# Performance work log

Measured on AMD Instinct MI355X. Metric: run time of the kernel, lower is better.

## Reference

```python
import jax, jax.numpy as jnp
import numpy as np

# Model dims (match init_kwargs / input_specs)
T, N, E, F_IN, F_OUT, BW = 16, 50000, 131072, 64, 64, 3


def setup_inputs() -> dict:
    key = jax.random.key(0)
    ks = jax.random.split(key, 6)
    x = jax.random.normal(ks[0], (T, N, F_IN), dtype=jnp.float32)
    M = jax.random.normal(ks[1], (T, T), dtype=jnp.float32)
    adj_rows = jax.random.randint(ks[2], (T, E), 0, N, dtype=jnp.int32)
    adj_cols = jax.random.randint(ks[3], (T, E), 0, N, dtype=jnp.int32)
    adj_vals = jax.random.uniform(ks[4], (T, E), dtype=jnp.float32)
    lim = float(np.sqrt(6.0 / (F_IN + F_OUT)))  # xavier_uniform
    weight = jax.random.uniform(ks[5], (F_IN, F_OUT), minval=-lim, maxval=lim, dtype=jnp.float32)
    return {"x": x, "M": M, "adj_vals": adj_vals, "weight": weight,
            "adj_rows": adj_rows, "adj_cols": adj_cols}


def _spmm(vals, rows, cols, x):
    # COO sparse [N,N] @ dense [N,F]: gather source rows, scatter-add to dest rows.
    return jax.ops.segment_sum(vals[:, None] * x[cols], rows, num_segments=x.shape[0])


def reference(x, M, adj_vals, weight, adj_rows, adj_cols):
    Tn, Nn, F = x.shape
    # Xt = M @ X (full M, as in compute_AtXt)
    Xt = (M @ x.reshape(Tn, -1)).reshape(Tn, Nn, F)
    k_idx = jnp.arange(Tn)
    AtXt = jnp.zeros((Tn, Nn, F), dtype=x.dtype)
    # Banded combination: At[k] = sum_{d=0}^{BW-1, k-d>=0} M[k, k-d] * A[k-d]
    # so At[k] @ Xt[k] = sum_d M[k,k-d] * (A[k-d] @ Xt[k])  -- avoids materializing At.
    for d in range(BW):
        j = k_idx - d
        valid = j >= 0
        jc = jnp.maximum(j, 0)
        w = jnp.where(valid, M[k_idx, jc], 0.0)  # [T] banded weights
        contrib = jax.vmap(_spmm)(adj_vals[jc], adj_rows[jc], adj_cols[jc], Xt)  # [T,N,F]
        AtXt = AtXt + w[:, None, None] * contrib
    # dropout is identity in eval mode; final dense projection
    return AtXt @ weight  # [T, N, F_OUT]
```

## Files before the change

kernel.cpp:

```cpp
#include <hip/hip_runtime.h>

#define TT 16
#define NN 50000
#define FF 64
#define EE 131072
#define NEDGE (TT*EE)
#define RPB 32
#define NRANGE ((NN + RPB - 1) / RPB)
#define NSUB 8
#define BCAP 256
#define NBUCK (NRANGE*NSUB)
#define SLOTS (NSUB*BCAP)
#define EMAX 1791
#define TAILI (EMAX*2)
#define APPBLKS (NEDGE/256)

typedef __attribute__((ext_vector_type(8))) short bf16x8;
typedef __attribute__((ext_vector_type(4))) short bf16x4;
typedef __attribute__((ext_vector_type(4))) float f32x4;
typedef __attribute__((ext_vector_type(2))) int   i32x2;
typedef __attribute__((ext_vector_type(2))) unsigned u32x2;

__device__ __forceinline__ unsigned pack2bf(float a, float b) {
    unsigned ua = __float_as_uint(a) + 0x8000u;
    unsigned ub = __float_as_uint(b) + 0x8000u;
    return __builtin_amdgcn_perm(ub, ua, 0x07060302u);
}
__device__ __forceinline__ float lo16f(unsigned u) { return __uint_as_float(u << 16); }
__device__ __forceinline__ float hi16f(unsigned u) { return __uint_as_float(u & 0xFFFF0000u); }

union U8 { unsigned u[4]; bf16x8 v; };
union U4 { unsigned u[2]; bf16x4 v; };

__device__ __forceinline__ f32x4 mfma16x16x16bf16(bf16x4 a, bf16x4 b, f32x4 c) {
#if __has_builtin(__builtin_amdgcn_mfma_f32_16x16x16bf16_1k)
    return __builtin_amdgcn_mfma_f32_16x16x16bf16_1k(a, b, c, 0, 0, 0);
#elif __has_builtin(__builtin_amdgcn_mfma_f32_16x16x16_bf16)
    return __builtin_amdgcn_mfma_f32_16x16x16_bf16(a, b, c, 0, 0, 0);
#else
    f32x4 d;
    asm volatile("v_mfma_f32_16x16x16_bf16 %0, %1, %2, %3\n\ts_nop 7\n\ts_nop 7"
                 : "=&v"(d) : "v"(a), "v"(b), "v"(c));
    return d;
#endif
}

__global__ __launch_bounds__(256) void k1_proj_mix(
    const float* __restrict__ x, const float* __restrict__ M,
    const float* __restrict__ W, unsigned short* __restrict__ Yt)
{
    const int tid  = threadIdx.x;
    const int wid  = tid >> 6;
    const int lane = tid & 63;
    const int col  = lane & 15;
    const int grp  = lane >> 4;

    bf16x8 bw[2][4];
#pragma unroll
    for (int q = 0; q < 2; ++q)
#pragma unroll
        for (int t = 0; t < 4; ++t) {
            U8 w8;
#pragma unroll
            for (int p = 0; p < 4; ++p)
                w8.u[p] = pack2bf(W[(q*32 + grp*8 + 2*p)*FF + t*16 + col],
                                  W[(q*32 + grp*8 + 2*p + 1)*FF + t*16 + col]);
            bw[q][t] = w8.v;
        }

    U4 m4;
    m4.u[0] = pack2bf(M[col*16 + grp*4 + 0], M[col*16 + grp*4 + 1]);
    m4.u[1] = pack2bf(M[col*16 + grp*4 + 2], M[col*16 + grp*4 + 3]);
    const bf16x4 mf = m4.v;

    const f32x4 zero = {0.f, 0.f, 0.f, 0.f};
    const int nwaves = gridDim.x * 4;

    for (int node = blockIdx.x*4 + wid; node < NN; node += nwaves) {
        const float* xb = x + (size_t)col*NN*FF + (size_t)node*FF + grp*8;
        float4 v0 = *reinterpret_cast<const float4*>(xb);
        float4 v1 = *reinterpret_cast<const float4*>(xb + 4);
        float4 v2 = *reinterpret_cast<const float4*>(xb + 32);
        float4 v3 = *reinterpret_cast<const float4*>(xb + 36);
        U8 a0, a1;
        a0.u[0] = pack2bf(v0.x, v0.y); a0.u[1] = pack2bf(v0.z, v0.w);
        a0.u[2] = pack2bf(v1.x, v1.y); a0.u[3] = pack2bf(v1.z, v1.w);
        a1.u[0] = pack2bf(v2.x, v2.y); a1.u[1] = pack2bf(v2.z, v2.w);
        a1.u[2] = pack2bf(v3.x, v3.y); a1.u[3] = pack2bf(v3.z, v3.w);

        f32x4 acc[4];
#pragma unroll
        for (int t = 0; t < 4; ++t) acc[t] = zero;
#pragma unroll
        for (int t = 0; t < 4; ++t)
            acc[t] = __builtin_amdgcn_mfma_f32_16x16x32_bf16(a0.v, bw[0][t], acc[t], 0, 0, 0);
#pragma unroll
        for (int t = 0; t < 4; ++t)
            acc[t] = __builtin_amdgcn_mfma_f32_16x16x32_bf16(a1.v, bw[1][t], acc[t], 0, 0, 0);

#pragma unroll
        for (int t = 0; t < 4; ++t) {
            U4 pb;
            pb.u[0] = pack2bf(acc[t][0], acc[t][1]);
            pb.u[1] = pack2bf(acc[t][2], acc[t][3]);
            f32x4 y = mfma16x16x16bf16(pb.v, mf, zero);
            u32x2 st;
            st[0] = pack2bf(y[0], y[1]);
            st[1] = pack2bf(y[2], y[3]);
            *reinterpret_cast<u32x2*>(Yt + (size_t)node*1024 + col*64 + t*16 + grp*4) = st;
        }
    }
}

__global__ __launch_bounds__(256) void append_kernel(
    const int* __restrict__ rows, const int* __restrict__ cols,
    const float* __restrict__ vals, int* __restrict__ bcnt,
    i32x2* __restrict__ btmp)
{
    const int i = blockIdx.x*256 + threadIdx.x;
    const int r = rows[i];
    const int j = i >> 17;
    const int b = (r >> 5)*NSUB + (blockIdx.x & 7);
    const int pos = atomicAdd(&bcnt[b], 1);
    if (pos < BCAP) {
        i32x2 e;
        e[0] = cols[i] | (((r & 31)*16 + j) << 16);
        e[1] = __float_as_int(vals[i]);
        btmp[(size_t)b*BCAP + pos] = e;
    }
}

__global__ __launch_bounds__(256) void sort_kernel(
    const int* __restrict__ bcnt, i32x2* __restrict__ btmp)
{
    __shared__ i32x2 sbuf[SLOTS];
    __shared__ int scnt[512], soff[512], scur[512], pscan[256];

    const int tid = threadIdx.x;
    const int blk = blockIdx.x;
    i32x2* region = btmp + (size_t)blk*SLOTS;

    scnt[tid] = 0; scnt[tid + 256] = 0;
    __syncthreads();

    int bc[NSUB]; i32x2 ent[NSUB];
#pragma unroll
    for (int s = 0; s < NSUB; ++s) {
        int c = bcnt[blk*NSUB + s];
        bc[s] = c < BCAP ? c : BCAP;
    }
#pragma unroll
    for (int s = 0; s < NSUB; ++s)
        if (tid < bc[s]) {
            ent[s] = region[s*BCAP + tid];
            atomicAdd(&scnt[((unsigned)ent[s][0]) >> 16], 1);
        }
    __syncthreads();

    const int a0 = scnt[2*tid], a1 = scnt[2*tid + 1];
    const int ps = a0 + a1;
    pscan[tid] = ps;
    __syncthreads();
    for (int o = 1; o < 256; o <<= 1) {
        int v = (tid >= o) ? pscan[tid - o] : 0;
        __syncthreads();
        pscan[tid] += v;
        __syncthreads();
    }
    const int excl = pscan[tid] - ps;
    soff[2*tid] = excl;      soff[2*tid + 1] = excl + a0;
    scur[2*tid] = excl;      scur[2*tid + 1] = excl + a0;
    __syncthreads();

#pragma unroll
    for (int s = 0; s < NSUB; ++s)
        if (tid < bc[s]) {
            const int key = ((unsigned)ent[s][0]) >> 16;
            const int pos = atomicAdd(&scur[key], 1);
            i32x2 se; se[0] = ent[s][0] & 0xFFFF; se[1] = ent[s][1];
            sbuf[pos] = se;
        }
    __syncthreads();

    const int total = soff[511] + scnt[511];
    const int lim = total < EMAX ? total : EMAX;
    for (int i = tid; i < lim; i += 256) region[i] = sbuf[i];
    int* tail = (int*)region + TAILI;
    tail[tid] = soff[tid];
    tail[tid + 256] = soff[tid + 256];
    if (tid == 0) tail[512] = lim;
}

template<int J>
__device__ __forceinline__ void k2_batch(int p0, int nj, int sbase, int esub, int fq,
    const i32x2* eb, const unsigned short* __restrict__ Yt,
    const float* __restrict__ M, f32x4* acc)
{
    const int p = p0 + esub;
    const bool act = p < nj;
    const int li = act ? (sbase + p) : 0;
    const i32x2 ent = eb[li];
    const float v = act ? __int_as_float(ent[1]) : 0.f;
    const int node = act ? ent[0] : 0;
    const unsigned short* yb = Yt + (size_t)node*1024 + J*64 + fq*4;
    {
        const u32x2 uv = *reinterpret_cast<const u32x2*>(yb);
        const float wv = M[J*17] * v;
        acc[J][0] = fmaf(wv, lo16f(uv[0]), acc[J][0]);
        acc[J][1] = fmaf(wv, hi16f(uv[0]), acc[J][1]);
        acc[J][2] = fmaf(wv, lo16f(uv[1]), acc[J][2]);
        acc[J][3] = fmaf(wv, hi16f(uv[1]), acc[J][3]);
    }
    if constexpr (J < 15) {
        const u32x2 uv = *reinterpret_cast<const u32x2*>(yb + 64);
        const float wv = M[J*17 + 16] * v;
        acc[J+1][0] = fmaf(wv, lo16f(uv[0]), acc[J+1][0]);
        acc[J+1][1] = fmaf(wv, hi16f(uv[0]), acc[J+1][1]);
        acc[J+1][2] = fmaf(wv, lo16f(uv[1]), acc[J+1][2]);
        acc[J+1][3] = fmaf(wv, hi16f(uv[1]), acc[J+1][3]);
    }
    if constexpr (J < 14) {
        const u32x2 uv = *reinterpret_cast<const u32x2*>(yb + 128);
        const float wv = M[J*17 + 32] * v;
        acc[J+2][0] = fmaf(wv, lo16f(uv[0]), acc[J+2][0]);
        acc[J+2][1] = fmaf(wv, hi16f(uv[0]), acc[J+2][1]);
        acc[J+2][2] = fmaf(wv, lo16f(uv[1]), acc[J+2][2]);
        acc[J+2][3] = fmaf(wv, hi16f(uv[1]), acc[J+2][3]);
    }
}

__global__ __launch_bounds__(256) void k2_gather(
    const unsigned short* __restrict__ Yt, const float* __restrict__ M,
    const i32x2* __restrict__ btmp, float* __restrict__ out)
{
    __shared__ i32x2 ebuf[4][128];
    const int tid  = threadIdx.x;
    const int wid  = tid >> 6;
    const int lane = tid & 63;
    const int esub = lane >> 4;
    const int fq   = lane & 15;
    const int r   = blockIdx.x*4 + wid;
    const int blk = r >> 5;
    const int rl  = r & 31;

    const i32x2* region = btmp + (size_t)blk*SLOTS;
    const int* tail = (const int*)region + TAILI;
    int o_l = 0;
    if (lane < 17) o_l = tail[rl*16 + lane];
    int off[17];
#pragma unroll
    for (int j = 0; j < 17; ++j) off[j] = __builtin_amdgcn_readlane(o_l, j);
    int ntot = off[16] - off[0];
    ntot = ntot < 128 ? ntot : 128;
    const i32x2* rowsrc = region + off[0];

    i32x2* eb = ebuf[wid];
    if (lane < ntot)      eb[lane]      = rowsrc[lane];
    if (lane + 64 < ntot) eb[lane + 64] = rowsrc[lane + 64];

    int c[16], sb[16];
#pragma unroll
    for (int j = 0; j < 16; ++j) {
        c[j]  = off[j+1] - off[j];
        sb[j] = off[j] - off[0];
    }

    f32x4 acc[16];
#pragma unroll
    for (int k = 0; k < 16; ++k) acc[k] = (f32x4){0.f, 0.f, 0.f, 0.f};

#define P1(J) k2_batch<J>(0, c[J], sb[J], esub, fq, eb, Yt, M, acc);
    P1(0)  P1(1)  P1(2)  P1(3)  P1(4)  P1(5)  P1(6)  P1(7)
    P1(8)  P1(9)  P1(10) P1(11) P1(12) P1(13) P1(14) P1(15)
#undef P1
#define P2(J) for (int p0 = 4; p0 < c[J]; p0 += 4) \
        k2_batch<J>(p0, c[J], sb[J], esub, fq, eb, Yt, M, acc);
    P2(0)  P2(1)  P2(2)  P2(3)  P2(4)  P2(5)  P2(6)  P2(7)
    P2(8)  P2(9)  P2(10) P2(11) P2(12) P2(13) P2(14) P2(15)
#undef P2

#pragma unroll
    for (int k = 0; k < 16; ++k) {
#pragma unroll
        for (int u = 0; u < 4; ++u) {
            acc[k][u] += __shfl_xor(acc[k][u], 16);
            acc[k][u] += __shfl_xor(acc[k][u], 32);
        }
    }
    if (esub == 0) {
#pragma unroll
        for (int k = 0; k < 16; ++k) {
            *reinterpret_cast<f32x4*>(out + ((size_t)k*NN + r)*FF + fq*4) = acc[k];
        }
    }
}

extern "C" void kernel_launch(void* const* d_in, const int* in_sizes, int n_in,
                              void* d_out, int out_size, void* d_ws, size_t ws_size,
                              hipStream_t stream) {
    (void)in_sizes; (void)n_in; (void)out_size; (void)ws_size;
    const float* x     = (const float*)d_in[0];
    const float* M     = (const float*)d_in[1];
    const float* avals = (const float*)d_in[2];
    const float* W     = (const float*)d_in[3];
    const int*   arows = (const int*)d_in[4];
    const int*   acols = (const int*)d_in[5];
    float* out = (float*)d_out;

    char* ws = (char*)d_ws;
    size_t o = 0;
    unsigned short* Yt = (unsigned short*)(ws + o); o += (size_t)TT*NN*FF*2;
    o = (o + 255) & ~(size_t)255;
    int* bcnt = (int*)(ws + o); o += (size_t)NBUCK*4;  o = (o + 255) & ~(size_t)255;
    i32x2* btmp = (i32x2*)(ws + o);

    (void)hipMemsetAsync(bcnt, 0, (size_t)NBUCK*4, stream);
    hipLaunchKernelGGL(k1_proj_mix, dim3(2048), dim3(256), 0, stream, x, M, W, Yt);
    hipLaunchKernelGGL(append_kernel, dim3(APPBLKS), dim3(256), 0, stream,
                       arows, acols, avals, bcnt, btmp);
    hipLaunchKernelGGL(sort_kernel, dim3(NRANGE), dim3(256), 0, stream, bcnt, btmp);
    hipLaunchKernelGGL(k2_gather, dim3(12500), dim3(256), 0, stream, Yt, M, btmp, out);
}
```

Measured before the change: 361.4 us.

## Fuse projection kernel with edge append and stage x tiles through swizzled LDS

Merges the projection/time-mix kernel and the edge-bucketing append kernel into one launch, with block index selecting the role, so the two independent stages can run at the same time on the GPU. The projection part now loads 8-node tiles across all 16 timesteps into double-buffered, XOR-swizzled LDS, giving coalesced global reads instead of strided per-lane loads. The aim is to remove one launch gap and improve memory efficiency. In exchange, the append blocks now carry the 32 KB LDS allocation, which can lower occupancy, and the grid is fixed at four tiles per block.

```diff
diff --git a/kernel.cpp b/kernel.cpp
--- a/kernel.cpp
+++ b/kernel.cpp
@@ -13,6 +13,8 @@
 #define SLOTS (NSUB*BCAP)
 #define EMAX 1791
 #define TAILI (EMAX*2)
+#define NTILES 6250
+#define K1BLKS 1563
 #define APPBLKS (NEDGE/256)
 
 typedef __attribute__((ext_vector_type(8))) short bf16x8;
@@ -45,88 +47,115 @@
 #endif
 }
 
-__global__ __launch_bounds__(256) void k1_proj_mix(
+__global__ void k1_append(
     const float* __restrict__ x, const float* __restrict__ M,
-    const float* __restrict__ W, unsigned short* __restrict__ Yt)
-{
-    const int tid  = threadIdx.x;
-    const int wid  = tid >> 6;
-    const int lane = tid & 63;
-    const int col  = lane & 15;
-    const int grp  = lane >> 4;
-
-    bf16x8 bw[2][4];
-#pragma unroll
-    for (int q = 0; q < 2; ++q)
-#pragma unroll
-        for (int t = 0; t < 4; ++t) {
-            U8 w8;
-#pragma unroll
-            for (int p = 0; p < 4; ++p)
-                w8.u[p] = pack2bf(W[(q*32 + grp*8 + 2*p)*FF + t*16 + col],
-                                  W[(q*32 + grp*8 + 2*p + 1)*FF + t*16 + col]);
-            bw[q][t] = w8.v;
-        }
-
-    U4 m4;
-    m4.u[0] = pack2bf(M[col*16 + grp*4 + 0], M[col*16 + grp*4 + 1]);
-    m4.u[1] = pack2bf(M[col*16 + grp*4 + 2], M[col*16 + grp*4 + 3]);
-    const bf16x4 mf = m4.v;
-
-    const f32x4 zero = {0.f, 0.f, 0.f, 0.f};
-    const int nwaves = gridDim.x * 4;
-
-    for (int node = blockIdx.x*4 + wid; node < NN; node += nwaves) {
-        const float* xb = x + (size_t)col*NN*FF + (size_t)node*FF + grp*8;
-        float4 v0 = *reinterpret_cast<const float4*>(xb);
-        float4 v1 = *reinterpret_cast<const float4*>(xb + 4);
-        float4 v2 = *reinterpret_cast<const float4*>(xb + 32);
-        float4 v3 = *reinterpret_cast<const float4*>(xb + 36);
-        U8 a0, a1;
-        a0.u[0] = pack2bf(v0.x, v0.y); a0.u[1] = pack2bf(v0.z, v0.w);
-        a0.u[2] = pack2bf(v1.x, v1.y); a0.u[3] = pack2bf(v1.z, v1.w);
-        a1.u[0] = pack2bf(v2.x, v2.y); a1.u[1] = pack2bf(v2.z, v2.w);
-        a1.u[2] = pack2bf(v3.x, v3.y); a1.u[3] = pack2bf(v3.z, v3.w);
-
-        f32x4 acc[4];
-#pragma unroll
-        for (int t = 0; t < 4; ++t) acc[t] = zero;
-#pragma unroll
-        for (int t = 0; t < 4; ++t)
-            acc[t] = __builtin_amdgcn_mfma_f32_16x16x32_bf16(a0.v, bw[0][t], acc[t], 0, 0, 0);
-#pragma unroll
-        for (int t = 0; t < 4; ++t)
-            acc[t] = __builtin_amdgcn_mfma_f32_16x16x32_bf16(a1.v, bw[1][t], acc[t], 0, 0, 0);
-
-#pragma unroll
-        for (int t = 0; t < 4; ++t) {
-            U4 pb;
-            pb.u[0] = pack2bf(acc[t][0], acc[t][1]);
-            pb.u[1] = pack2bf(acc[t][2], acc[t][3]);
-            f32x4 y = mfma16x16x16bf16(pb.v, mf, zero);
-            u32x2 st;
-            st[0] = pack2bf(y[0], y[1]);
-            st[1] = pack2bf(y[2], y[3]);
-            *reinterpret_cast<u32x2*>(Yt + (size_t)node*1024 + col*64 + t*16 + grp*4) = st;
-        }
-    }
-}
-
-__global__ __launch_bounds__(256) void append_kernel(
+    const float* __restrict__ W, unsigned short* __restrict__ Yt,
     const int* __restrict__ rows, const int* __restrict__ cols,
     const float* __restrict__ vals, int* __restrict__ bcnt,
     i32x2* __restrict__ btmp)
 {
-    const int i = blockIdx.x*256 + threadIdx.x;
-    const int r = rows[i];
-    const int j = i >> 17;
-    const int b = (r >> 5)*NSUB + (blockIdx.x & 7);
-    const int pos = atomicAdd(&bcnt[b], 1);
-    if (pos < BCAP) {
-        i32x2 e;
-        e[0] = cols[i] | (((r & 31)*16 + j) << 16);
-        e[1] = __float_as_int(vals[i]);
-        btmp[(size_t)b*BCAP + pos] = e;
+    __shared__ __align__(16) char lds[2][16384];
+
+    if (blockIdx.x < K1BLKS) {
+        const int tid  = threadIdx.x;
+        const int wid  = tid >> 6;
+        const int lane = tid & 63;
+        const int col  = lane & 15;
+        const int grp  = lane >> 4;
+
+        bf16x8 bw[2][4];
+#pragma unroll
+        for (int q = 0; q < 2; ++q)
+#pragma unroll
+            for (int t = 0; t < 4; ++t) {
+                U8 w8;
+#pragma unroll
+                for (int p = 0; p < 4; ++p)
+                    w8.u[p] = pack2bf(W[(q*32 + grp*8 + 2*p)*FF + t*16 + col],
+                                      W[(q*32 + grp*8 + 2*p + 1)*FF + t*16 + col]);
+                bw[q][t] = w8.v;
+            }
+
+        U4 m4;
+        m4.u[0] = pack2bf(M[col*16 + grp*4 + 0], M[col*16 + grp*4 + 1]);
+        m4.u[1] = pack2bf(M[col*16 + grp*4 + 2], M[col*16 + grp*4 + 3]);
+        const bf16x4 mf = m4.v;
+        const f32x4 zero = {0.f, 0.f, 0.f, 0.f};
+
+#define STAGE(tt, buf)                                                        \
+        {                                                                     \
+            const int nb_ = (tt)*8;                                           \
+            char* L_ = lds[buf];                                              \
+            _Pragma("unroll")                                                 \
+            for (int q = 0; q < 4; ++q) {                                     \
+                const int s_ = wid*4 + q;                                     \
+                const float* src_ = x + (size_t)s_*NN*FF + (size_t)nb_*FF + lane*8; \
+                float4 lo_ = *reinterpret_cast<const float4*>(src_);          \
+                float4 hi_ = *reinterpret_cast<const float4*>(src_ + 4);      \
+                U8 pk_;                                                       \
+                pk_.u[0] = pack2bf(lo_.x, lo_.y); pk_.u[1] = pack2bf(lo_.z, lo_.w); \
+                pk_.u[2] = pack2bf(hi_.x, hi_.y); pk_.u[3] = pack2bf(hi_.z, hi_.w); \
+                const int byte_ = (s_*1024 + lane*16) ^ ((s_ & 7) << 4);      \
+                *reinterpret_cast<bf16x8*>(L_ + byte_) = pk_.v;               \
+            }                                                                 \
+        }
+
+        const int t0 = blockIdx.x*4;
+        if (t0 < NTILES) STAGE(t0, 0)
+
+#pragma unroll
+        for (int i = 0; i < 4; ++i) {
+            const int t = t0 + i;
+            if (t >= NTILES) break;
+            __syncthreads();
+            if (i + 1 < 4 && t + 1 < NTILES) STAGE(t + 1, (i + 1) & 1)
+
+            const char* L = lds[i & 1];
+#pragma unroll
+            for (int h = 0; h < 2; ++h) {
+                const int nloc = wid*2 + h;
+                const int node = t*8 + nloc;
+                const int base = (col*1024 + nloc*128) ;
+                const int sw = (col & 7) << 4;
+                bf16x8 a0 = *reinterpret_cast<const bf16x8*>(L + ((base + grp*16) ^ sw));
+                bf16x8 a1 = *reinterpret_cast<const bf16x8*>(L + ((base + 64 + grp*16) ^ sw));
+
+                f32x4 acc[4];
+#pragma unroll
+                for (int t2 = 0; t2 < 4; ++t2) acc[t2] = zero;
+#pragma unroll
+                for (int t2 = 0; t2 < 4; ++t2)
+                    acc[t2] = __builtin_amdgcn_mfma_f32_16x16x32_bf16(a0, bw[0][t2], acc[t2], 0, 0, 0);
+#pragma unroll
+                for (int t2 = 0; t2 < 4; ++t2)
+                    acc[t2] = __builtin_amdgcn_mfma_f32_16x16x32_bf16(a1, bw[1][t2], acc[t2], 0, 0, 0);
+
+#pragma unroll
+                for (int t2 = 0; t2 < 4; ++t2) {
+                    U4 pb;
+                    pb.u[0] = pack2bf(acc[t2][0], acc[t2][1]);
+                    pb.u[1] = pack2bf(acc[t2][2], acc[t2][3]);
+                    f32x4 y = mfma16x16x16bf16(pb.v, mf, zero);
+                    u32x2 st;
+                    st[0] = pack2bf(y[0], y[1]);
+                    st[1] = pack2bf(y[2], y[3]);
+                    *reinterpret_cast<u32x2*>(Yt + (size_t)node*1024 + col*64 + t2*16 + grp*4) = st;
+                }
+            }
+        }
+#undef STAGE
+    } else {
+        const int i = (blockIdx.x - K1BLKS)*256 + threadIdx.x;
+        const int r = rows[i];
+        const int j = i >> 17;
+        const int b = (r >> 5)*NSUB + (blockIdx.x & 7);
+        const int pos = atomicAdd(&bcnt[b], 1);
+        if (pos < BCAP) {
+            i32x2 e;
+            e[0] = cols[i] | (((r & 31)*16 + j) << 16);
+            e[1] = __float_as_int(vals[i]);
+            btmp[(size_t)b*BCAP + pos] = e;
+        }
     }
 }
 
@@ -315,9 +344,8 @@
     i32x2* btmp = (i32x2*)(ws + o);
 
     (void)hipMemsetAsync(bcnt, 0, (size_t)NBUCK*4, stream);
-    hipLaunchKernelGGL(k1_proj_mix, dim3(2048), dim3(256), 0, stream, x, M, W, Yt);
-    hipLaunchKernelGGL(append_kernel, dim3(APPBLKS), dim3(256), 0, stream,
-                       arows, acols, avals, bcnt, btmp);
+    hipLaunchKernelGGL(k1_append, dim3(K1BLKS + APPBLKS), dim3(256), 0, stream,
+                       x, M, W, Yt, arows, acols, avals, bcnt, btmp);
     hipLaunchKernelGGL(sort_kernel, dim3(NRANGE), dim3(256), 0, stream, bcnt, btmp);
     hipLaunchKernelGGL(k2_gather, dim3(12500), dim3(256), 0, stream, Yt, M, btmp, out);
 }
```

Result: faster. 329.4 us (-8.8%).
